# Performance work log

Measured on AMD Instinct MI355X. Metric: run time of the kernel, lower is better.

The kernel has to match this reference:

```python
import jax, jax.numpy as jnp
import numpy as np

N = 40000          # nodes
E = 1280000        # edges (avg degree 32)
S = 64             # num_scalars
V = 16             # num_vectors
R = 32             # num_radial
CUTOFF = 10.0


def setup_inputs() -> dict:
    key = jax.random.key(0)
    ks = jax.random.split(key, 12)
    scalars = jax.random.normal(ks[0], (N, S), dtype=jnp.float32)
    vectors = jax.random.normal(ks[1], (N, V, 3), dtype=jnp.float32)
    edge_index = jax.random.randint(ks[2], (2, E), 0, N, dtype=jnp.int64)
    edge_vec = jax.random.normal(ks[3], (E, 3), dtype=jnp.float32)
    # radial_net: Linear(R,R) -> SiLU -> Linear(R, S + 2V)
    W1 = jax.random.normal(ks[4], (R, R), dtype=jnp.float32) * 0.1
    b1 = jnp.zeros((R,), dtype=jnp.float32)
    W2 = jax.random.normal(ks[5], (R, S + 2 * V), dtype=jnp.float32) * 0.1
    b2 = jnp.zeros((S + 2 * V,), dtype=jnp.float32)
    # attention: Linear(2S+R, S) -> SiLU -> Linear(S, 1)
    Wa1 = jax.random.normal(ks[6], (2 * S + R, S), dtype=jnp.float32) * 0.1
    ba1 = jnp.zeros((S,), dtype=jnp.float32)
    Wa2 = jax.random.normal(ks[7], (S, 1), dtype=jnp.float32) * 0.1
    ba2 = jnp.zeros((1,), dtype=jnp.float32)
    return dict(scalars=scalars, vectors=vectors, edge_vec=edge_vec,
                W1=W1, b1=b1, W2=W2, b2=b2,
                Wa1=Wa1, ba1=ba1, Wa2=Wa2, ba2=ba2,
                edge_index=edge_index)


def reference(scalars, vectors, edge_vec, W1, b1, W2, b2, Wa1, ba1, Wa2, ba2, edge_index):
    src = edge_index[0]  # j (source)
    dst = edge_index[1]  # i (target / aggregation index)

    d = jnp.linalg.norm(edge_vec, axis=-1)                 # [E]
    d_safe = jnp.clip(d[:, None], 1e-8, None)              # [E,1]

    # Bessel radial basis with cosine cutoff
    freqs = (jnp.arange(1, R + 1, dtype=jnp.float32) * np.pi / CUTOFF)
    bessel = jnp.sin(freqs * d[:, None]) / d_safe          # [E,R]
    cut = 0.5 * (jnp.cos(np.pi * d[:, None] / CUTOFF) + 1.0)
    cut = cut * (d[:, None] < CUTOFF).astype(jnp.float32)
    rbf = bessel * cut                                     # [E,R]

    # spherical harmonics (lmax=1); vector already normalized, sh = [1, y, z, x]
    unit = edge_vec / d_safe                               # [E,3]
    sh_weight = jnp.stack([unit[:, 1], unit[:, 2], unit[:, 0]], axis=-1)  # [E,3]

    # radial filter MLP
    filters = jax.nn.silu(rbf @ W1 + b1) @ W2 + b2         # [E, S+2V]
    scalar_filter = filters[:, :S]
    vector_filter = filters[:, S:S + V]
    vector_gate = filters[:, S + V:]

    s_i = scalars[dst]                                     # [E,S]
    s_j = scalars[src]                                     # [E,S]
    v_j = vectors[src]                                     # [E,V,3]

    scalar_message = s_j * scalar_filter                   # [E,S]
    vector_message = (v_j * vector_filter[:, :, None]
                      + vector_gate[:, :, None] * sh_weight[:, None, :])  # [E,V,3]

    att_in = jnp.concatenate([s_i, s_j, rbf], axis=-1)     # [E, 2S+R]
    att = jax.nn.sigmoid(jax.nn.silu(att_in @ Wa1 + ba1) @ Wa2 + ba2)  # [E,1]

    scalar_message = att * scalar_message
    vector_message = att[:, :, None] * vector_message

    scalar_aggr = jax.ops.segment_sum(scalar_message, dst, num_segments=N)
    vector_aggr = jax.ops.segment_sum(vector_message, dst, num_segments=N)

    return scalars + scalar_aggr, vectors + vector_aggr
```

## Files before the change

kernel.cpp:

```cpp
#include <hip/hip_runtime.h>

static constexpr int N_ = 40000;
static constexpr int E_ = 1280000;
static constexpr int NS = N_ * 64;
static constexpr int NV = N_ * 48;

typedef _Float16 half2_t __attribute__((ext_vector_type(2)));
typedef _Float16 half8_t __attribute__((ext_vector_type(8)));
typedef float float4_t __attribute__((ext_vector_type(4)));
typedef unsigned int uint;

__device__ __forceinline__ float silu_f(float x) { return __fdividef(x, 1.f + __expf(-x)); }
__device__ __forceinline__ int rfl(int x) { return __builtin_amdgcn_readfirstlane(x); }

__global__ __launch_bounds__(256) void k_front1(
    const int* __restrict__ eidx, int* __restrict__ cntp, int* __restrict__ rnk,
    const float* __restrict__ scalars, const float* __restrict__ vectors,
    _Float16* __restrict__ sc16p, _Float16* __restrict__ vec16p,
    const float* __restrict__ W1, const float* __restrict__ Wa1,
    const float* __restrict__ W2, uint* __restrict__ tbl, uint* __restrict__ tbl2)
{
    int bid = blockIdx.x;
    if (bid < 1250) {
        int base = bid * 1024 + threadIdx.x;
#pragma unroll
        for (int k = 0; k < 4; k++) {
            int e = base + k * 256;
            rnk[e] = atomicAdd(&cntp[eidx[E_ + e] * 16], 1);
        }
        return;
    }
    if (bid < 6250) {
        int t = (bid - 1250) * 256 + threadIdx.x;
        if (t < N_ * 16) {
            int n = t >> 4, bl = t & 15;
            const float* srow = scalars + (size_t)n * 64;
            half2_t a, b;
            a.x = (_Float16)srow[bl];
            a.y = (_Float16)srow[16 + bl];
            b.x = (_Float16)srow[32 + bl];
            b.y = (_Float16)srow[48 + bl];
            uint2 u; u.x = __builtin_bit_cast(uint, a); u.y = __builtin_bit_cast(uint, b);
            *(uint2*)(sc16p + (size_t)n * 64 + bl * 4) = u;
        } else {
            int tt = t - N_ * 16;
            int n = tt >> 4, bl = tt & 15;
            const float* vrow = vectors + (size_t)n * 48 + bl * 3;
            half2_t a, b;
            a.x = (_Float16)vrow[0];
            a.y = (_Float16)vrow[1];
            b.x = (_Float16)vrow[2];
            b.y = (_Float16)0.f;
            uint2 u; u.x = __builtin_bit_cast(uint, a); u.y = __builtin_bit_cast(uint, b);
            *(uint2*)(vec16p + (size_t)n * 64 + bl * 4) = u;
        }
        return;
    }
    int t = (bid - 6250) * 256 + threadIdx.x;
    if (t < 1536) {
        int j = t >> 4, q = t & 15;
        int k0 = 2 * q, k1 = 2 * q + 1;
        float a = (j < 64) ? Wa1[(128 + k0) * 64 + j] : W1[k0 * 32 + (j - 64)];
        float b = (j < 64) ? Wa1[(128 + k1) * 64 + j] : W1[k1 * 32 + (j - 64)];
        half2_t v; v.x = (_Float16)a; v.y = (_Float16)b;
        tbl[t] = __builtin_bit_cast(uint, v);
    } else if (t < 3072) {
        int tt = t - 1536;
        int j = tt >> 4, q = tt & 15;
        half2_t v;
        v.x = (_Float16)W2[(2 * q + 0) * 96 + j];
        v.y = (_Float16)W2[(2 * q + 1) * 96 + j];
        tbl2[tt] = __builtin_bit_cast(uint, v);
    }
}

static constexpr int PATT_BLOCKS = 512;
__global__ __launch_bounds__(256) void k_patt(
    const float* __restrict__ scalars, const float* __restrict__ Wa1,
    const float* __restrict__ ba1,
    _Float16* __restrict__ P1h, _Float16* __restrict__ P2h)
{
    int gw   = (blockIdx.x * 256 + threadIdx.x) >> 6;
    int lane = threadIdx.x & 63;
    float w[128];
#pragma unroll
    for (int k = 0; k < 128; k++) w[k] = Wa1[k * 64 + lane];
    float bias = ba1[lane];
    for (int n = gw; n < N_; n += PATT_BLOCKS * 4) {
        float sv = scalars[(size_t)n * 64 + lane];
        float a1 = bias, a2 = 0.f;
#pragma unroll
        for (int k = 0; k < 64; k++) {
            float sk = __shfl(sv, k, 64);
            a1 = fmaf(sk, w[k], a1);
            a2 = fmaf(sk, w[64 + k], a2);
        }
        P1h[(size_t)n * 64 + lane] = (_Float16)a1;
        P2h[(size_t)n * 64 + lane] = (_Float16)a2;
    }
}

__global__ void k_scan1(const int* __restrict__ cntp, int* __restrict__ row_start,
                        int* __restrict__ bsum)
{
    __shared__ int buf[1024];
    int b = blockIdx.x, tid = threadIdx.x;
    int idx = b * 1024 + tid;
    int v = (idx < N_) ? cntp[idx * 16] : 0;
    buf[tid] = v;
    __syncthreads();
    for (int off = 1; off < 1024; off <<= 1) {
        int t = (tid >= off) ? buf[tid - off] : 0;
        __syncthreads();
        buf[tid] += t;
        __syncthreads();
    }
    if (idx < N_) row_start[idx] = buf[tid] - v;
    if (tid == 1023) bsum[b] = buf[1023];
}

__global__ void k_scan3(const int* __restrict__ bsum, int* __restrict__ row_start)
{
    __shared__ int boffs;
    if (threadIdx.x == 0) {
        int s = 0;
        for (int b = 0; b < (int)blockIdx.x; b++) s += bsum[b];
        boffs = s;
    }
    __syncthreads();
    int idx = blockIdx.x * 1024 + threadIdx.x;
    if (idx < N_) row_start[idx] += boffs;
    if (idx == N_) row_start[N_] = E_;
}

__global__ void k_place3(const int* __restrict__ eidx, const float* __restrict__ edge_vec,
                         const int* __restrict__ row_start, const int* __restrict__ r,
                         float4* __restrict__ rec)
{
    int e = blockIdx.x * 256 + threadIdx.x;
    int src = eidx[e];
    int dst = eidx[E_ + e];
    size_t slot = (size_t)(row_start[dst] + r[e]);
    uint sd = (uint)src | ((uint)dst << 16);
    rec[slot] = make_float4(edge_vec[3 * e + 0], edge_vec[3 * e + 1],
                            edge_vec[3 * e + 2], __uint_as_float(sd));
}

__global__ __launch_bounds__(256, 3) void k_edges_sorted(
    const float4* __restrict__ rec,
    const _Float16* __restrict__ P1h, const _Float16* __restrict__ P2h,
    const uint* __restrict__ tbl, const float* __restrict__ b1,
    const float* __restrict__ Wa2, const float* __restrict__ ba2,
    float4* __restrict__ attsh, int* __restrict__ srcbuf, uint* __restrict__ hbufp)
{
    __shared__ char lds_raw[4 * 8448];
    int tid = threadIdx.x;
    int wid = tid >> 6, lane = tid & 63;
    char* wbase = lds_raw + wid * 8448;
    int bl = lane & 15, bq = lane >> 4;

    int i = blockIdx.x * 256 + tid;
    float4 ra = rec[(size_t)i];
    float ev0 = ra.x, ev1 = ra.y, ev2 = ra.z;
    uint sd = __float_as_uint(ra.w);
    int src = (int)(sd & 0xffffu);
    int dst = (int)(sd >> 16);

    float d = sqrtf(fmaf(ev0, ev0, fmaf(ev1, ev1, ev2 * ev2)));
    float inv_d = __fdividef(1.f, fmaxf(d, 1e-8f));
    float cut = (d < 10.f) ? 0.5f * (__cosf(0.31415927f * d) + 1.f) : 0.f;
    float cutd = cut * inv_d;
    float sh0 = ev1 * inv_d, sh1 = ev2 * inv_d, sh2 = ev0 * inv_d;

    float th = 0.31415927f * d;
    float scur = __sinf(th);
    float twoC = 2.f * __cosf(th);
    float sprev = 0.f;
    uint rbf2[16];
#pragma unroll
    for (int q = 0; q < 16; q++) {
        float r0 = scur * cutd;
        float snext = fmaf(twoC, scur, -sprev);
        sprev = scur; scur = snext;
        float r1 = scur * cutd;
        snext = fmaf(twoC, scur, -sprev);
        sprev = scur; scur = snext;
        half2_t v; v.x = (_Float16)r0; v.y = (_Float16)r1;
        rbf2[q] = __builtin_bit_cast(uint, v);
    }
    {
        uint4* rw = (uint4*)(wbase + lane * 64);
        rw[0] = make_uint4(rbf2[0], rbf2[1], rbf2[2], rbf2[3]);
        rw[1] = make_uint4(rbf2[4], rbf2[5], rbf2[6], rbf2[7]);
        rw[2] = make_uint4(rbf2[8], rbf2[9], rbf2[10], rbf2[11]);
        rw[3] = make_uint4(rbf2[12], rbf2[13], rbf2[14], rbf2[15]);
    }
    uint4 bfr[6];
#pragma unroll
    for (int u = 0; u < 6; u++)
        bfr[u] = *(const uint4*)(tbl + (u * 16 + bl) * 16 + bq * 4);

    uint4 afr[4];
#pragma unroll
    for (int t = 0; t < 4; t++)
        afr[t] = *(const uint4*)(wbase + (t * 16 + bl) * 64 + bq * 16);

    _Float16* gtile = (_Float16*)wbase;

#pragma unroll
    for (int t = 0; t < 4; t++) {
        half8_t av = __builtin_bit_cast(half8_t, afr[t]);
        int eb = t * 16 + bq * 4;
#pragma unroll
        for (int u = 4; u < 6; u++) {
            float4_t dd = __builtin_amdgcn_mfma_f32_16x16x32_f16(
                av, __builtin_bit_cast(half8_t, bfr[u]), (float4_t)(0.f), 0, 0, 0);
            int col = (u - 4) * 16 + bl;
            gtile[(eb + 0) * 34 + col] = (_Float16)dd[0];
            gtile[(eb + 1) * 34 + col] = (_Float16)dd[1];
            gtile[(eb + 2) * 34 + col] = (_Float16)dd[2];
            gtile[(eb + 3) * 34 + col] = (_Float16)dd[3];
        }
    }
    {
        const uint* growB = (const uint*)(wbase + (size_t)lane * 68);
        uint hp[16];
#pragma unroll
        for (int q = 0; q < 16; q++) {
            half2_t gg = __builtin_bit_cast(half2_t, growB[q]);
            half2_t v;
            v.x = (_Float16)silu_f((float)gg.x + b1[2 * q + 0]);
            v.y = (_Float16)silu_f((float)gg.y + b1[2 * q + 1]);
            hp[q] = __builtin_bit_cast(uint, v);
        }
        uint4* hrow4 = (uint4*)(hbufp + (size_t)i * 16);
#pragma unroll
        for (int q = 0; q < 4; q++)
            hrow4[q] = make_uint4(hp[4 * q + 0], hp[4 * q + 1], hp[4 * q + 2], hp[4 * q + 3]);
    }

#pragma unroll
    for (int t = 0; t < 4; t++) {
        half8_t av = __builtin_bit_cast(half8_t, afr[t]);
        int eb = t * 16 + bq * 4;
#pragma unroll
        for (int u = 0; u < 4; u++) {
            float4_t dd = __builtin_amdgcn_mfma_f32_16x16x32_f16(
                av, __builtin_bit_cast(half8_t, bfr[u]), (float4_t)(0.f), 0, 0, 0);
            int col = u * 16 + bl;
            gtile[(eb + 0) * 66 + col] = (_Float16)dd[0];
            gtile[(eb + 1) * 66 + col] = (_Float16)dd[1];
            gtile[(eb + 2) * 66 + col] = (_Float16)dd[2];
            gtile[(eb + 3) * 66 + col] = (_Float16)dd[3];
        }
    }
    const uint* grow = (const uint*)(wbase + (size_t)lane * 132);

    const uint2* p1h = (const uint2*)(P1h + (size_t)dst * 64);
    const uint2* p2h = (const uint2*)(P2h + (size_t)src * 64);
    float logit = ba2[0];
#pragma unroll
    for (int q = 0; q < 16; q++) {
        uint2 ua = p1h[q];
        uint2 ub = p2h[q];
        half2_t s01 = __builtin_bit_cast(half2_t, ua.x) + __builtin_bit_cast(half2_t, ub.x)
                    + __builtin_bit_cast(half2_t, grow[2 * q + 0]);
        half2_t s23 = __builtin_bit_cast(half2_t, ua.y) + __builtin_bit_cast(half2_t, ub.y)
                    + __builtin_bit_cast(half2_t, grow[2 * q + 1]);
        logit = fmaf(silu_f((float)s01.x), Wa2[4 * q + 0], logit);
        logit = fmaf(silu_f((float)s01.y), Wa2[4 * q + 1], logit);
        logit = fmaf(silu_f((float)s23.x), Wa2[4 * q + 2], logit);
        logit = fmaf(silu_f((float)s23.y), Wa2[4 * q + 3], logit);
    }
    float att = __fdividef(1.f, 1.f + __expf(-logit));

    attsh[i] = make_float4(att, sh0, sh1, sh2);
    srcbuf[i] = src;
}

static constexpr int NPW = 5;
__global__ __launch_bounds__(256, 4) void k_gather_mfma(
    const float* __restrict__ scalars, const float* __restrict__ vectors,
    const _Float16* __restrict__ sc16p, const _Float16* __restrict__ vec16p,
    const float* __restrict__ b2,
    const int* __restrict__ row_start,
    const float4* __restrict__ attsh, const int* __restrict__ srcbuf,
    const uint* __restrict__ hbuf, const uint* __restrict__ tbl2,
    float* __restrict__ out)
{
    int wid  = threadIdx.x >> 6;
    int lane = threadIdx.x & 63;
    int gw   = blockIdx.x * 4 + wid;
    int bl = lane & 15, bq = lane >> 4;

    uint4 bfr2[6];
#pragma unroll
    for (int u = 0; u < 6; u++)
        bfr2[u] = *(const uint4*)(tbl2 + (u * 16 + bl) * 16 + bq * 4);

    float b2s[4];
#pragma unroll
    for (int u = 0; u < 4; u++) b2s[u] = b2[u * 16 + bl];
    float bvf = b2[64 + bl], bvg = b2[80 + bl];

    int n0 = gw * NPW;
    for (int nn = 0; nn < NPW; nn++) {
        int n = n0 + nn;
        int rs = rfl(row_start[n]);
        int re = rfl(row_start[n + 1]);

        float accS0 = 0.f, accS1 = 0.f, accS2 = 0.f, accS3 = 0.f;
        float accV0 = 0.f, accV1 = 0.f, accV2 = 0.f;

        for (int i0 = rs; i0 < re; i0 += 16) {
            uint4 av4 = make_uint4(0u, 0u, 0u, 0u);
            if (i0 + bl < re)
                av4 = *(const uint4*)(hbuf + (size_t)(i0 + bl) * 16 + bq * 4);
            half8_t av = __builtin_bit_cast(half8_t, av4);

            float4_t d0 = __builtin_amdgcn_mfma_f32_16x16x32_f16(av, __builtin_bit_cast(half8_t, bfr2[0]), (float4_t)(0.f), 0, 0, 0);
            float4_t d1 = __builtin_amdgcn_mfma_f32_16x16x32_f16(av, __builtin_bit_cast(half8_t, bfr2[1]), (float4_t)(0.f), 0, 0, 0);
            float4_t d2 = __builtin_amdgcn_mfma_f32_16x16x32_f16(av, __builtin_bit_cast(half8_t, bfr2[2]), (float4_t)(0.f), 0, 0, 0);
            float4_t d3 = __builtin_amdgcn_mfma_f32_16x16x32_f16(av, __builtin_bit_cast(half8_t, bfr2[3]), (float4_t)(0.f), 0, 0, 0);
            float4_t d4 = __builtin_amdgcn_mfma_f32_16x16x32_f16(av, __builtin_bit_cast(half8_t, bfr2[4]), (float4_t)(0.f), 0, 0, 0);
            float4_t d5 = __builtin_amdgcn_mfma_f32_16x16x32_f16(av, __builtin_bit_cast(half8_t, bfr2[5]), (float4_t)(0.f), 0, 0, 0);

#pragma unroll
            for (int r = 0; r < 4; r++) {
                int slot = i0 + bq * 4 + r;
                int ok = (slot < re);
                int cs = ok ? slot : (re - 1);
                float4 as = attsh[cs];
                float att = ok ? as.x : 0.f;
                int src = srcbuf[cs];
                uint2 su = *(const uint2*)(sc16p + (size_t)src * 64 + bl * 4);
                uint2 vu = *(const uint2*)(vec16p + (size_t)src * 64 + bl * 4);
                half2_t s01 = __builtin_bit_cast(half2_t, su.x);
                half2_t s23 = __builtin_bit_cast(half2_t, su.y);
                half2_t v01 = __builtin_bit_cast(half2_t, vu.x);
                half2_t v23 = __builtin_bit_cast(half2_t, vu.y);
                accS0 = fmaf(att * (float)s01.x, d0[r] + b2s[0], accS0);
                accS1 = fmaf(att * (float)s01.y, d1[r] + b2s[1], accS1);
                accS2 = fmaf(att * (float)s23.x, d2[r] + b2s[2], accS2);
                accS3 = fmaf(att * (float)s23.y, d3[r] + b2s[3], accS3);
                float vf = d4[r] + bvf;
                float vg = d5[r] + bvg;
                accV0 = fmaf(att, fmaf((float)v01.x, vf, vg * as.y), accV0);
                accV1 = fmaf(att, fmaf((float)v01.y, vf, vg * as.z), accV1);
                accV2 = fmaf(att, fmaf((float)v23.x, vf, vg * as.w), accV2);
            }
        }

        accS0 += __shfl_xor(accS0, 16, 64); accS0 += __shfl_xor(accS0, 32, 64);
        accS1 += __shfl_xor(accS1, 16, 64); accS1 += __shfl_xor(accS1, 32, 64);
        accS2 += __shfl_xor(accS2, 16, 64); accS2 += __shfl_xor(accS2, 32, 64);
        accS3 += __shfl_xor(accS3, 16, 64); accS3 += __shfl_xor(accS3, 32, 64);
        accV0 += __shfl_xor(accV0, 16, 64); accV0 += __shfl_xor(accV0, 32, 64);
        accV1 += __shfl_xor(accV1, 16, 64); accV1 += __shfl_xor(accV1, 32, 64);
        accV2 += __shfl_xor(accV2, 16, 64); accV2 += __shfl_xor(accV2, 32, 64);

        if (bq == 0) {
            size_t o = (size_t)n * 64 + bl;
            out[o +  0] = scalars[o +  0] + accS0;
            out[o + 16] = scalars[o + 16] + accS1;
            out[o + 32] = scalars[o + 32] + accS2;
            out[o + 48] = scalars[o + 48] + accS3;
            size_t ov = (size_t)n * 48 + 3 * bl;
            out[NS + ov + 0] = vectors[ov + 0] + accV0;
            out[NS + ov + 1] = vectors[ov + 1] + accV1;
            out[NS + ov + 2] = vectors[ov + 2] + accV2;
        }
    }
}

extern "C" void kernel_launch(void* const* d_in, const int* in_sizes, int n_in,
                              void* d_out, int out_size, void* d_ws, size_t ws_size,
                              hipStream_t stream)
{
    const float* scalars  = (const float*)d_in[0];
    const float* vectors  = (const float*)d_in[1];
    const float* edge_vec = (const float*)d_in[2];
    const float* W1  = (const float*)d_in[3];
    const float* b1  = (const float*)d_in[4];
    const float* W2  = (const float*)d_in[5];
    const float* b2  = (const float*)d_in[6];
    const float* Wa1 = (const float*)d_in[7];
    const float* ba1 = (const float*)d_in[8];
    const float* Wa2 = (const float*)d_in[9];
    const float* ba2 = (const float*)d_in[10];
    const int* eidx  = (const int*)d_in[11];

    char* wsb = (char*)d_ws;
    float4* attsh = (float4*)wsb;
    float*  P1    = (float*)(wsb + (size_t)E_ * 16);
    float*  P2    = P1 + NS;
    float*  hbuf  = P2 + NS;
    int* cnt       = (int*)(hbuf + (size_t)32 * E_);
    int* bsum      = cnt + N_;
    int* row_start = cnt + 2 * N_;
    int* perm      = row_start + N_ + 1;
    int* srcbuf    = perm + E_;
    int*  rnk  = (int*)hbuf;
    uint* tbl  = (uint*)hbuf + (size_t)16 * E_;
    uint* tbl2 = tbl + 1536;
    _Float16* P1h  = (_Float16*)(tbl2 + 1536);
    _Float16* P2h  = P1h + NS;
    _Float16* sc16p = P2h + NS;
    _Float16* vec16p = (_Float16*)P1;
    float4* rec = (float4*)(sc16p + NS);
    int* cntp   = (int*)(rec + E_);

    hipMemsetAsync(cntp, 0, (size_t)N_ * 16 * sizeof(int), stream);
    k_front1<<<6262, 256, 0, stream>>>(eidx, cntp, rnk, scalars, vectors,
                                       sc16p, vec16p, W1, Wa1, W2, tbl, tbl2);
    k_scan1<<<40, 1024, 0, stream>>>(cntp, row_start, bsum);
    k_scan3<<<40, 1024, 0, stream>>>(bsum, row_start);
    k_place3<<<5000, 256, 0, stream>>>(eidx, edge_vec, row_start, rnk, rec);
    k_patt<<<PATT_BLOCKS, 256, 0, stream>>>(scalars, Wa1, ba1, P1h, P2h);
    k_edges_sorted<<<5000, 256, 0, stream>>>(rec, P1h, P2h,
                                             tbl, b1, Wa2, ba2,
                                             attsh, srcbuf, (uint*)hbuf);
    k_gather_mfma<<<2000, 256, 0, stream>>>(scalars, vectors, sc16p, vec16p, b2, row_start,
                                            attsh, srcbuf, (const uint*)hbuf, tbl2,
                                            (float*)d_out);
}
```

Measured before the change: 358.3 us.

## Privatize per-destination edge counters per XCC to avoid cross-die atomics

Result: slower. 388.6 us (+8.4%).

```diff
diff --git a/kernel.cpp b/kernel.cpp
--- a/kernel.cpp
+++ b/kernel.cpp
@@ -12,9 +12,14 @@
 
 __device__ __forceinline__ float silu_f(float x) { return __fdividef(x, 1.f + __expf(-x)); }
 __device__ __forceinline__ int rfl(int x) { return __builtin_amdgcn_readfirstlane(x); }
+__device__ __forceinline__ int xcc_id() {
+    int x;
+    asm volatile("s_getreg_b32 %0, hwreg(HW_REG_XCC_ID)" : "=s"(x));
+    return x & 7;
+}
 
 __global__ __launch_bounds__(256) void k_front1(
-    const int* __restrict__ eidx, int* __restrict__ cntp, int* __restrict__ rnk,
+    const int* __restrict__ eidx, int* __restrict__ cnt8, int* __restrict__ rnk,
     const float* __restrict__ scalars, const float* __restrict__ vectors,
     _Float16* __restrict__ sc16p, _Float16* __restrict__ vec16p,
     const float* __restrict__ W1, const float* __restrict__ Wa1,
@@ -22,11 +27,14 @@
 {
     int bid = blockIdx.x;
     if (bid < 1250) {
+        int c = xcc_id();
         int base = bid * 1024 + threadIdx.x;
 #pragma unroll
         for (int k = 0; k < 4; k++) {
             int e = base + k * 256;
-            rnk[e] = atomicAdd(&cntp[eidx[E_ + e] * 16], 1);
+            int dst = eidx[E_ + e];
+            int r = atomicAdd(&cnt8[((size_t)dst * 8 + c) * 16], 1);
+            rnk[e] = (c << 24) | r;
         }
         return;
     }
@@ -100,13 +108,20 @@
     }
 }
 
-__global__ void k_scan1(const int* __restrict__ cntp, int* __restrict__ row_start,
-                        int* __restrict__ bsum)
+__global__ void k_scan1(const int* __restrict__ cnt8, int* __restrict__ pre8,
+                        int* __restrict__ row_start, int* __restrict__ bsum)
 {
     __shared__ int buf[1024];
     int b = blockIdx.x, tid = threadIdx.x;
     int idx = b * 1024 + tid;
-    int v = (idx < N_) ? cntp[idx * 16] : 0;
+    int v = 0;
+    if (idx < N_) {
+#pragma unroll
+        for (int c = 0; c < 8; c++) {
+            pre8[idx * 8 + c] = v;
+            v += cnt8[((size_t)idx * 8 + c) * 16];
+        }
+    }
     buf[tid] = v;
     __syncthreads();
     for (int off = 1; off < 1024; off <<= 1) {
@@ -134,13 +149,15 @@
 }
 
 __global__ void k_place3(const int* __restrict__ eidx, const float* __restrict__ edge_vec,
-                         const int* __restrict__ row_start, const int* __restrict__ r,
-                         float4* __restrict__ rec)
+                         const int* __restrict__ row_start, const int* __restrict__ pre8,
+                         const int* __restrict__ r, float4* __restrict__ rec)
 {
     int e = blockIdx.x * 256 + threadIdx.x;
     int src = eidx[e];
     int dst = eidx[E_ + e];
-    size_t slot = (size_t)(row_start[dst] + r[e]);
+    int rc = r[e];
+    int c = rc >> 24, rr = rc & 0xffffff;
+    size_t slot = (size_t)(row_start[dst] + pre8[dst * 8 + c] + rr);
     uint sd = (uint)src | ((uint)dst << 16);
     rec[slot] = make_float4(edge_vec[3 * e + 0], edge_vec[3 * e + 1],
                             edge_vec[3 * e + 2], __uint_as_float(sd));
@@ -408,14 +425,15 @@
     _Float16* sc16p = P2h + NS;
     _Float16* vec16p = (_Float16*)P1;
     float4* rec = (float4*)(sc16p + NS);
-    int* cntp   = (int*)(rec + E_);
-
-    hipMemsetAsync(cntp, 0, (size_t)N_ * 16 * sizeof(int), stream);
-    k_front1<<<6262, 256, 0, stream>>>(eidx, cntp, rnk, scalars, vectors,
+    int* cnt8   = (int*)(rec + E_);
+    int* pre8   = cnt8 + (size_t)N_ * 8 * 16;
+
+    hipMemsetAsync(cnt8, 0, (size_t)N_ * 8 * 16 * sizeof(int), stream);
+    k_front1<<<6262, 256, 0, stream>>>(eidx, cnt8, rnk, scalars, vectors,
                                        sc16p, vec16p, W1, Wa1, W2, tbl, tbl2);
-    k_scan1<<<40, 1024, 0, stream>>>(cntp, row_start, bsum);
+    k_scan1<<<40, 1024, 0, stream>>>(cnt8, pre8, row_start, bsum);
     k_scan3<<<40, 1024, 0, stream>>>(bsum, row_start);
-    k_place3<<<5000, 256, 0, stream>>>(eidx, edge_vec, row_start, rnk, rec);
+    k_place3<<<5000, 256, 0, stream>>>(eidx, edge_vec, row_start, pre8, rnk, rec);
     k_patt<<<PATT_BLOCKS, 256, 0, stream>>>(scalars, Wa1, ba1, P1h, P2h);
     k_edges_sorted<<<5000, 256, 0, stream>>>(rec, P1h, P2h,
                                              tbl, b1, Wa2, ba2,
```
